# Kernel optimization log

Hardware: AMD Instinct MI355X
Metric: run time of the kernel (lower is better)

## Reference

```python
import jax, jax.numpy as jnp
import numpy as np

B, T, C = 2, 2048, 1024
NH = 16

def setup_inputs() -> dict:
    key = jax.random.key(0)
    ks = jax.random.split(key, 5)
    s = 0.02
    return {
        "x": jax.random.normal(ks[0], (B, T, C), dtype=jnp.float32),
        "w_attn": jax.random.normal(ks[1], (C, 3 * C), dtype=jnp.float32) * s,
        "b_attn": jax.random.normal(ks[2], (3 * C,), dtype=jnp.float32) * s,
        "w_proj": jax.random.normal(ks[3], (C, C), dtype=jnp.float32) * s,
        "b_proj": jax.random.normal(ks[4], (C,), dtype=jnp.float32) * s,
        "n_heads": NH,
    }

def reference(x, w_attn, b_attn, w_proj, b_proj, n_heads):
    Bx, Tx, Cx = x.shape
    hd = Cx // n_heads
    qkv = x @ w_attn + b_attn                      # [B,T,3C]
    q, k, v = jnp.split(qkv, 3, axis=-1)
    # [B,T,H,hd] -> [B,H,T,hd]
    q = q.reshape(Bx, Tx, n_heads, hd).transpose(0, 2, 1, 3)
    k = k.reshape(Bx, Tx, n_heads, hd).transpose(0, 2, 1, 3)
    v = v.reshape(Bx, Tx, n_heads, hd).transpose(0, 2, 1, 3)
    scale = 1.0 / np.sqrt(hd).astype(np.float32)
    att = jnp.einsum('bhqd,bhkd->bhqk', q, k) * scale   # [B,H,T,T]
    causal = jnp.tril(jnp.ones((Tx, Tx), dtype=bool))
    att = jnp.where(causal[None, None], att, -jnp.inf)
    att = jax.nn.softmax(att, axis=-1)
    y = jnp.einsum('bhqk,bhkd->bhqd', att, v)            # [B,H,T,hd]
    y = y.transpose(0, 2, 1, 3).reshape(Bx, Tx, Cx)
    return y @ w_proj + b_proj
```

## Files before the change

kernel.cpp:

```cpp
#include <hip/hip_runtime.h>

typedef __bf16 bf16x8 __attribute__((ext_vector_type(8)));
typedef __bf16 bf16x4 __attribute__((ext_vector_type(4)));
typedef float  f32x4  __attribute__((ext_vector_type(4)));

#define MFMA_BF16(a, b, c) __builtin_amdgcn_mfma_f32_16x16x32_bf16((a), (b), (c), 0, 0, 0)
#define NEG_INF (-1e30f)
#define SCL 0.18033688f

__device__ __forceinline__ void gld16(const void* g, void* l) {
  __builtin_amdgcn_global_load_lds(
      (const __attribute__((address_space(1))) void*)g,
      (__attribute__((address_space(3))) void*)l, 16, 0, 0);
}

__global__ void cast_f32_bf16(const float* __restrict__ in,
                              __bf16* __restrict__ out, int n) {
  int i = (blockIdx.x * 256 + threadIdx.x) * 8;
  if (i >= n) return;
  float4 a = *(const float4*)&in[i];
  float4 b = *(const float4*)&in[i + 4];
  bf16x8 v;
  v[0] = (__bf16)a.x; v[1] = (__bf16)a.y; v[2] = (__bf16)a.z; v[3] = (__bf16)a.w;
  v[4] = (__bf16)b.x; v[5] = (__bf16)b.y; v[6] = (__bf16)b.z; v[7] = (__bf16)b.w;
  *(bf16x8*)&out[i] = v;
}

__global__ void transpose_f32_bf16(const float* __restrict__ in,
                                   __bf16* __restrict__ out, int R, int C) {
  __shared__ float t[32][33];
  int tx = threadIdx.x & 31, ty = threadIdx.x >> 5;
  int x = blockIdx.x * 32 + tx;
  int y0 = blockIdx.y * 32 + ty;
#pragma unroll
  for (int i = 0; i < 4; ++i)
    t[ty + 8 * i][tx] = in[(size_t)(y0 + 8 * i) * C + x];
  __syncthreads();
  int x2 = blockIdx.y * 32 + tx;
#pragma unroll
  for (int i = 0; i < 4; ++i)
    out[(size_t)(blockIdx.x * 32 + ty + 8 * i) * R + x2] = (__bf16)t[tx][ty + 8 * i];
}

#define BN 128
#define BK 64

template <int BMT, typename TC>
__global__ __launch_bounds__(256) void gemm_bt_bias(
    const __bf16* __restrict__ A, const __bf16* __restrict__ Bt,
    const float* __restrict__ bias, TC* __restrict__ Cmat,
    int M, int N, int K) {
  constexpr int NI = BMT / 32;
  __shared__ __align__(16) __bf16 As[BMT * BK];
  __shared__ __align__(16) __bf16 Bs[BN * BK];
  int tid = threadIdx.x;
  int wave = tid >> 6, lane = tid & 63;
  int l16 = lane & 15, quad = lane >> 4;
  int wm = wave >> 1, wn = wave & 1;
  int m0 = blockIdx.y * BMT, n0 = blockIdx.x * BN;

  f32x4 acc[NI][4];
#pragma unroll
  for (int i = 0; i < NI; ++i)
#pragma unroll
    for (int j = 0; j < 4; ++j) acc[i][j] = (f32x4){0.f, 0.f, 0.f, 0.f};

  int row = tid >> 3;
  int kc = ((tid & 7) ^ ((tid >> 3) & 7)) * 8;
  int xr = (l16 & 7) * 8;

  for (int k0 = 0; k0 < K; k0 += BK) {
#pragma unroll
    for (int i = 0; i < NI; ++i)
      gld16(&A[(size_t)(m0 + row + i * 32) * K + k0 + kc],
            (char*)As + (i * 256 + wave * 64) * 16);
#pragma unroll
    for (int j = 0; j < 4; ++j)
      gld16(&Bt[(size_t)(n0 + row + j * 32) * K + k0 + kc],
            (char*)Bs + (j * 256 + wave * 64) * 16);
    __syncthreads();
#pragma unroll
    for (int ks = 0; ks < 2; ++ks) {
      bf16x8 af[NI], bfr[4];
#pragma unroll
      for (int i = 0; i < NI; ++i)
        af[i] = *(const bf16x8*)&As[(wm * (BMT / 2) + i * 16 + l16) * BK +
                                    ((ks * 32 + quad * 8) ^ xr)];
#pragma unroll
      for (int j = 0; j < 4; ++j)
        bfr[j] = *(const bf16x8*)&Bs[(wn * 64 + j * 16 + l16) * BK +
                                     ((ks * 32 + quad * 8) ^ xr)];
#pragma unroll
      for (int i = 0; i < NI; ++i)
#pragma unroll
        for (int j = 0; j < 4; ++j) acc[i][j] = MFMA_BF16(af[i], bfr[j], acc[i][j]);
    }
    __syncthreads();
  }
#pragma unroll
  for (int i = 0; i < NI; ++i) {
#pragma unroll
    for (int j = 0; j < 4; ++j) {
      int col = n0 + wn * 64 + j * 16 + l16;
      float bv = bias[col];
#pragma unroll
      for (int r = 0; r < 4; ++r) {
        int rw = m0 + wm * (BMT / 2) + i * 16 + quad * 4 + r;
        Cmat[(size_t)rw * N + col] = (TC)(acc[i][j][r] + bv);
      }
    }
  }
}

__global__ __launch_bounds__(256) void attn_causal(
    const __bf16* __restrict__ qkv, __bf16* __restrict__ y) {
  __shared__ __align__(16) __bf16 Kb[2][64 * 64];
  __shared__ __align__(16) __bf16 Vb[2][64 * 72];
  __shared__ __align__(16) __bf16 Ps[4][16 * 72];
  const int tid = threadIdx.x;
  const int wave = tid >> 6, lane = tid & 63;
  const int l16 = lane & 15, quad = lane >> 4;
  const int bh = blockIdx.x;
  const int b = bh >> 4, h = bh & 15;
  const int RS = 3072;

  const int key0 = tid >> 3;
  const int d0 = (tid & 7) * 8;
  const int kcs = ((tid & 7) ^ ((tid >> 3) & 7)) * 8;
  const int xr = (l16 & 7) * 8;
  const __bf16* kbase = qkv + (size_t)(b * 2048) * RS + 1024 + h * 64 + kcs;
  const __bf16* vbase = qkv + (size_t)(b * 2048) * RS + 2048 + h * 64 + d0;

#pragma unroll 1
  for (int phase = 0; phase < 2; ++phase) {
    const int qt = phase ? (31 - (int)blockIdx.y) : (int)blockIdx.y;

    int qrow = b * 2048 + qt * 64 + wave * 16 + l16;
    const __bf16* qbase = qkv + (size_t)qrow * RS + h * 64;
    bf16x8 qf0 = *(const bf16x8*)(qbase + quad * 8);
    bf16x8 qf1 = *(const bf16x8*)(qbase + 32 + quad * 8);

    float l_i = 0.f;
    f32x4 o[4];
#pragma unroll
    for (int j = 0; j < 4; ++j) o[j] = (f32x4){0.f, 0.f, 0.f, 0.f};

    bf16x8 vreg[2];
#pragma unroll
    for (int i = 0; i < 2; ++i) {
      gld16(kbase + (size_t)(key0 + 32 * i) * RS,
            (char*)Kb[0] + (i * 256 + tid) * 16);
      vreg[i] = *(const bf16x8*)(vbase + (size_t)(key0 + 32 * i) * RS);
    }
#pragma unroll
    for (int i = 0; i < 2; ++i) {
      int key = key0 + 32 * i;
#pragma unroll
      for (int jj = 0; jj < 8; ++jj)
        Vb[0][(d0 + jj) * 72 + (key ^ d0)] = vreg[i][jj];
    }
    __syncthreads();

    for (int kt = 0; kt <= qt; ++kt) {
      const int cur = kt & 1;
      if (kt < qt) {
#pragma unroll
        for (int i = 0; i < 2; ++i) {
          gld16(kbase + (size_t)((kt + 1) * 64 + key0 + 32 * i) * RS,
                (char*)Kb[cur ^ 1] + (i * 256 + tid) * 16);
          vreg[i] = *(const bf16x8*)(vbase + (size_t)((kt + 1) * 64 + key0 + 32 * i) * RS);
        }
      }

      f32x4 s[4];
#pragma unroll
      for (int j = 0; j < 4; ++j) s[j] = (f32x4){0.f, 0.f, 0.f, 0.f};
#pragma unroll
      for (int j = 0; j < 4; ++j) {
        bf16x8 kf0 = *(const bf16x8*)&Kb[cur][(j * 16 + l16) * 64 + ((quad * 8) ^ xr)];
        bf16x8 kf1 = *(const bf16x8*)&Kb[cur][(j * 16 + l16) * 64 + ((32 + quad * 8) ^ xr)];
        s[j] = MFMA_BF16(kf0, qf0, s[j]);
        s[j] = MFMA_BF16(kf1, qf1, s[j]);
      }

      if (kt == qt) {
        int qg = wave * 16 + l16;
#pragma unroll
        for (int j = 0; j < 4; ++j)
#pragma unroll
          for (int r = 0; r < 4; ++r)
            if (j * 16 + quad * 4 + r > qg) s[j][r] = NEG_INF;
      }

#pragma unroll
      for (int j = 0; j < 4; ++j) {
        bf16x4 pb;
#pragma unroll
        for (int r = 0; r < 4; ++r) {
          float p = __builtin_amdgcn_exp2f(s[j][r] * SCL);
          l_i += p;
          pb[r] = (__bf16)p;
        }
        *(bf16x4*)&Ps[wave][l16 * 72 + j * 16 + quad * 4] = pb;
      }

#pragma unroll
      for (int ks = 0; ks < 2; ++ks) {
        bf16x8 pf = *(const bf16x8*)&Ps[wave][l16 * 72 + ks * 32 + quad * 8];
#pragma unroll
        for (int j = 0; j < 4; ++j) {
          int dim = j * 16 + l16;
          bf16x8 vf = *(const bf16x8*)&Vb[cur][dim * 72 + ((ks * 32 + quad * 8) ^ (dim & 56))];
          o[j] = MFMA_BF16(pf, vf, o[j]);
        }
      }

      if (kt < qt) {
#pragma unroll
        for (int i = 0; i < 2; ++i) {
          int key = key0 + 32 * i;
#pragma unroll
          for (int jj = 0; jj < 8; ++jj)
            Vb[cur ^ 1][(d0 + jj) * 72 + (key ^ d0)] = vreg[i][jj];
        }
      }
      __syncthreads();
    }

    float lred = l_i;
    lred += __shfl_xor(lred, 16);
    lred += __shfl_xor(lred, 32);
    int orow = b * 2048 + qt * 64 + wave * 16 + quad * 4;
#pragma unroll
    for (int r = 0; r < 4; ++r) {
      float inv = 1.f / __shfl(lred, quad * 4 + r);
#pragma unroll
      for (int j = 0; j < 4; ++j)
        y[(size_t)(orow + r) * 1024 + h * 64 + j * 16 + l16] = (__bf16)(o[j][r] * inv);
    }
  }
}

extern "C" void kernel_launch(void* const* d_in, const int* in_sizes, int n_in,
                              void* d_out, int out_size, void* d_ws, size_t ws_size,
                              hipStream_t stream) {
  (void)in_sizes; (void)n_in; (void)out_size; (void)ws_size;
  const float* x      = (const float*)d_in[0];
  const float* w_attn = (const float*)d_in[1];
  const float* b_attn = (const float*)d_in[2];
  const float* w_proj = (const float*)d_in[3];
  const float* b_proj = (const float*)d_in[4];
  float* out = (float*)d_out;

  __bf16* wt_attn = (__bf16*)d_ws;
  __bf16* wt_proj = wt_attn + (size_t)3072 * 1024;
  __bf16* qkv     = wt_proj + (size_t)1024 * 1024;
  __bf16* ybuf    = qkv + (size_t)4096 * 3072;

  cast_f32_bf16<<<4096 * 1024 / 2048, 256, 0, stream>>>(x, ybuf, 4096 * 1024);

  transpose_f32_bf16<<<dim3(3072 / 32, 1024 / 32), 256, 0, stream>>>(w_attn, wt_attn, 1024, 3072);
  transpose_f32_bf16<<<dim3(1024 / 32, 1024 / 32), 256, 0, stream>>>(w_proj, wt_proj, 1024, 1024);

  gemm_bt_bias<128, __bf16><<<dim3(3072 / BN, 4096 / 128), 256, 0, stream>>>(
      ybuf, wt_attn, b_attn, qkv, 4096, 3072, 1024);

  attn_causal<<<dim3(2 * 16, 16), 256, 0, stream>>>(qkv, ybuf);

  gemm_bt_bias<64, float><<<dim3(1024 / BN, 4096 / 64), 256, 0, stream>>>(
      ybuf, wt_proj, b_proj, out, 4096, 1024, 1024);
}
```

Before: 180.2 us.

## Pre-transpose V into a separate buffer and load it via async LDS copies

```diff
diff --git a/kernel.cpp b/kernel.cpp
--- a/kernel.cpp
+++ b/kernel.cpp
@@ -40,6 +40,22 @@
 #pragma unroll
   for (int i = 0; i < 4; ++i)
     out[(size_t)(blockIdx.x * 32 + ty + 8 * i) * R + x2] = (__bf16)t[tx][ty + 8 * i];
+}
+
+__global__ void transpose_v(const __bf16* __restrict__ qkv,
+                            __bf16* __restrict__ vt) {
+  __shared__ __bf16 t[32][33];
+  int tx = threadIdx.x & 31, ty = threadIdx.x >> 5;
+  int bh = blockIdx.z, b = bh >> 4, h = bh & 15;
+  int t0 = blockIdx.x * 32, d0 = blockIdx.y * 32;
+#pragma unroll
+  for (int i = 0; i < 4; ++i)
+    t[ty + 8 * i][tx] =
+        qkv[(size_t)(b * 2048 + t0 + ty + 8 * i) * 3072 + 2048 + h * 64 + d0 + tx];
+  __syncthreads();
+#pragma unroll
+  for (int i = 0; i < 4; ++i)
+    vt[(size_t)(bh * 64 + d0 + ty + 8 * i) * 2048 + t0 + tx] = t[tx][ty + 8 * i];
 }
 
 #define BN 128
@@ -113,9 +129,10 @@
 }
 
 __global__ __launch_bounds__(256) void attn_causal(
-    const __bf16* __restrict__ qkv, __bf16* __restrict__ y) {
+    const __bf16* __restrict__ qkv, const __bf16* __restrict__ vt,
+    __bf16* __restrict__ y) {
   __shared__ __align__(16) __bf16 Kb[2][64 * 64];
-  __shared__ __align__(16) __bf16 Vb[2][64 * 72];
+  __shared__ __align__(16) __bf16 Vb[2][64 * 64];
   __shared__ __align__(16) __bf16 Ps[4][16 * 72];
   const int tid = threadIdx.x;
   const int wave = tid >> 6, lane = tid & 63;
@@ -124,12 +141,11 @@
   const int b = bh >> 4, h = bh & 15;
   const int RS = 3072;
 
-  const int key0 = tid >> 3;
-  const int d0 = (tid & 7) * 8;
+  const int row0 = tid >> 3;
   const int kcs = ((tid & 7) ^ ((tid >> 3) & 7)) * 8;
   const int xr = (l16 & 7) * 8;
   const __bf16* kbase = qkv + (size_t)(b * 2048) * RS + 1024 + h * 64 + kcs;
-  const __bf16* vbase = qkv + (size_t)(b * 2048) * RS + 2048 + h * 64 + d0;
+  const __bf16* vbase = vt + (size_t)(bh * 64) * 2048 + kcs;
 
 #pragma unroll 1
   for (int phase = 0; phase < 2; ++phase) {
@@ -145,19 +161,12 @@
 #pragma unroll
     for (int j = 0; j < 4; ++j) o[j] = (f32x4){0.f, 0.f, 0.f, 0.f};
 
-    bf16x8 vreg[2];
 #pragma unroll
     for (int i = 0; i < 2; ++i) {
-      gld16(kbase + (size_t)(key0 + 32 * i) * RS,
+      gld16(kbase + (size_t)(row0 + 32 * i) * RS,
             (char*)Kb[0] + (i * 256 + tid) * 16);
-      vreg[i] = *(const bf16x8*)(vbase + (size_t)(key0 + 32 * i) * RS);
-    }
-#pragma unroll
-    for (int i = 0; i < 2; ++i) {
-      int key = key0 + 32 * i;
-#pragma unroll
-      for (int jj = 0; jj < 8; ++jj)
-        Vb[0][(d0 + jj) * 72 + (key ^ d0)] = vreg[i][jj];
+      gld16(vbase + (size_t)(row0 + 32 * i) * 2048,
+            (char*)Vb[0] + (i * 256 + tid) * 16);
     }
     __syncthreads();
 
@@ -166,9 +175,10 @@
       if (kt < qt) {
 #pragma unroll
         for (int i = 0; i < 2; ++i) {
-          gld16(kbase + (size_t)((kt + 1) * 64 + key0 + 32 * i) * RS,
+          gld16(kbase + (size_t)((kt + 1) * 64 + row0 + 32 * i) * RS,
                 (char*)Kb[cur ^ 1] + (i * 256 + tid) * 16);
-          vreg[i] = *(const bf16x8*)(vbase + (size_t)((kt + 1) * 64 + key0 + 32 * i) * RS);
+          gld16(vbase + (size_t)(row0 + 32 * i) * 2048 + (kt + 1) * 64,
+                (char*)Vb[cur ^ 1] + (i * 256 + tid) * 16);
         }
       }
 
@@ -209,19 +219,9 @@
         bf16x8 pf = *(const bf16x8*)&Ps[wave][l16 * 72 + ks * 32 + quad * 8];
 #pragma unroll
         for (int j = 0; j < 4; ++j) {
-          int dim = j * 16 + l16;
-          bf16x8 vf = *(const bf16x8*)&Vb[cur][dim * 72 + ((ks * 32 + quad * 8) ^ (dim & 56))];
+          bf16x8 vf = *(const bf16x8*)&Vb[cur][(j * 16 + l16) * 64 +
+                                              ((ks * 32 + quad * 8) ^ xr)];
           o[j] = MFMA_BF16(pf, vf, o[j]);
-        }
-      }
-
-      if (kt < qt) {
-#pragma unroll
-        for (int i = 0; i < 2; ++i) {
-          int key = key0 + 32 * i;
-#pragma unroll
-          for (int jj = 0; jj < 8; ++jj)
-            Vb[cur ^ 1][(d0 + jj) * 72 + (key ^ d0)] = vreg[i][jj];
         }
       }
       __syncthreads();
@@ -256,6 +256,7 @@
   __bf16* wt_proj = wt_attn + (size_t)3072 * 1024;
   __bf16* qkv     = wt_proj + (size_t)1024 * 1024;
   __bf16* ybuf    = qkv + (size_t)4096 * 3072;
+  __bf16* vtbuf   = ybuf + (size_t)4096 * 1024;
 
   cast_f32_bf16<<<4096 * 1024 / 2048, 256, 0, stream>>>(x, ybuf, 4096 * 1024);
 
@@ -265,7 +266,9 @@
   gemm_bt_bias<128, __bf16><<<dim3(3072 / BN, 4096 / 128), 256, 0, stream>>>(
       ybuf, wt_attn, b_attn, qkv, 4096, 3072, 1024);
 
-  attn_causal<<<dim3(2 * 16, 16), 256, 0, stream>>>(qkv, ybuf);
+  transpose_v<<<dim3(64, 2, 32), 256, 0, stream>>>(qkv, vtbuf);
+
+  attn_causal<<<dim3(2 * 16, 16), 256, 0, stream>>>(qkv, vtbuf, ybuf);
 
   gemm_bt_bias<64, float><<<dim3(1024 / BN, 4096 / 64), 256, 0, stream>>>(
       ybuf, wt_proj, b_proj, out, 4096, 1024, 1024);
```

After: 179.5 us. No clear change (-0.4%).
